# Performance work log

Measured on AMD Instinct MI355X. Metric: run time of the kernel, lower is better.

The kernel has to match this reference:

```python
import jax, jax.numpy as jnp
import numpy as np

N, E, D, H, C, G, L = 100000, 1600000, 128, 4, 32, 4096, 3  # nodes, edges, h_dim, heads, head_dim, graphs, conv blocks


def setup_inputs() -> dict:
    key = jax.random.key(0)
    ks = jax.random.split(key, 24)
    s = 0.05
    w = lambda k, shape: jax.random.normal(k, shape, jnp.float32) * s
    inp = {
        "x": jax.random.normal(ks[0], (N, D), jnp.float32),
        "edge_index": jax.random.randint(ks[1], (2, E), 0, N),
        "batch": jnp.sort(jax.random.randint(ks[2], (N,), 0, G)),
        # input TransformerConv (in=D, out=C per head, H heads, beta=True)
        "in_Wq": w(ks[3], (D, D)), "in_bq": jnp.zeros((D,), jnp.float32),
        "in_Wk": w(ks[4], (D, D)), "in_bk": jnp.zeros((D,), jnp.float32),
        "in_Wv": w(ks[5], (D, D)), "in_bv": jnp.zeros((D,), jnp.float32),
        "in_Ws": w(ks[6], (D, D)), "in_bs": jnp.zeros((D,), jnp.float32),
        "in_Wbeta": w(ks[7], (3 * D,)),
        # stacked conv blocks (L of them, in=out=D)
        "blk_Wq": w(ks[8], (L, D, D)), "blk_bq": jnp.zeros((L, D), jnp.float32),
        "blk_Wk": w(ks[9], (L, D, D)), "blk_bk": jnp.zeros((L, D), jnp.float32),
        "blk_Wv": w(ks[10], (L, D, D)), "blk_bv": jnp.zeros((L, D), jnp.float32),
        "blk_Ws": w(ks[11], (L, D, D)), "blk_bs": jnp.zeros((L, D), jnp.float32),
        "blk_Wbeta": w(ks[12], (L, 3 * D)),
        # MLP head
        "W1": w(ks[13], (D, 64)), "b1": jnp.zeros((64,), jnp.float32),
        "W2": w(ks[14], (64, 32)), "b2": jnp.zeros((32,), jnp.float32),
        "W3": w(ks[15], (32, 1)), "b3": jnp.zeros((1,), jnp.float32),
    }
    return inp


def transformer_conv(x, src, dst, Wq, bq, Wk, bk, Wv, bv, Ws, bs, Wbeta):
    # PyG TransformerConv, concat=True, root_weight=True, beta=True, eval mode
    q = (x @ Wq + bq).reshape(N, H, C)
    k = (x @ Wk + bk).reshape(N, H, C)
    v = (x @ Wv + bv).reshape(N, H, C)
    # per-edge attention logits: message j=src -> i=dst
    alpha = jnp.einsum("ehc,ehc->eh", q[dst], k[src]) / jnp.sqrt(jnp.float32(C))  # [E,H]
    m = jax.ops.segment_max(alpha, dst, num_segments=N)
    m = jnp.where(jnp.isfinite(m), m, 0.0)
    e = jnp.exp(alpha - m[dst])
    denom = jax.ops.segment_sum(e, dst, num_segments=N)
    a = e / (denom[dst] + 1e-16)  # segment softmax over in-edges of dst
    msg = a[..., None] * v[src]  # [E,H,C]
    out = jax.ops.segment_sum(msg, dst, num_segments=N).reshape(N, H * C)
    x_r = x @ Ws + bs
    beta = jax.nn.sigmoid(jnp.concatenate([out, x_r, out - x_r], axis=-1) @ Wbeta)[:, None]
    return beta * x_r + (1.0 - beta) * out


def reference(x, edge_index, batch, in_Wq, in_bq, in_Wk, in_bk, in_Wv, in_bv,
              in_Ws, in_bs, in_Wbeta, blk_Wq, blk_bq, blk_Wk, blk_bk, blk_Wv,
              blk_bv, blk_Ws, blk_bs, blk_Wbeta, W1, b1, W2, b2, W3, b3):
    src, dst = edge_index[0], edge_index[1]
    h = jax.nn.relu(transformer_conv(x, src, dst, in_Wq, in_bq, in_Wk, in_bk,
                                     in_Wv, in_bv, in_Ws, in_bs, in_Wbeta))
    for l in range(L):  # dropout is identity in eval mode
        h = jax.nn.relu(transformer_conv(h, src, dst, blk_Wq[l], blk_bq[l],
                                         blk_Wk[l], blk_bk[l], blk_Wv[l], blk_bv[l],
                                         blk_Ws[l], blk_bs[l], blk_Wbeta[l]))
    # global mean pool over graphs
    sums = jax.ops.segment_sum(h, batch, num_segments=G)
    cnt = jax.ops.segment_sum(jnp.ones((N, 1), h.dtype), batch, num_segments=G)
    g = sums / jnp.maximum(cnt, 1.0)
    g = jax.nn.relu(g @ W1 + b1)
    g = jax.nn.relu(g @ W2 + b2)
    return jax.nn.sigmoid(g @ W3 + b3)
```

## Files before the change

### kernel.cpp

```cpp
#include <hip/hip_runtime.h>
#include <hip/hip_bf16.h>
#include <cstdint>

#define DH 128
#define NB 256
#define NBK 1024

typedef __attribute__((ext_vector_type(8))) short short8;
typedef __attribute__((ext_vector_type(4))) float floatx4;
typedef __attribute__((ext_vector_type(2))) float floatx2;

__device__ __forceinline__ float bflo(unsigned u) { return __uint_as_float(u << 16); }
__device__ __forceinline__ float bfhi(unsigned u) { return __uint_as_float(u & 0xffff0000u); }

__device__ __forceinline__ unsigned pk_bf16(float a, float b) {
  return ((unsigned)__bfloat16_as_ushort(__float2bfloat16(b)) << 16)
       | (unsigned)__bfloat16_as_ushort(__float2bfloat16(a));
}

template<int CTRL>
__device__ __forceinline__ float dpp_add(float x) {
  int y = __builtin_amdgcn_update_dpp(0, __float_as_int(x), CTRL, 0xf, 0xf, true);
  return x + __int_as_float(y);
}


__global__ void zero_i32(int* __restrict__ p, int n) {
  int i = blockIdx.x * 256 + threadIdx.x;
  if (i < n) p[i] = 0;
}


__global__ void cvt_bf16(const float* __restrict__ x, __hip_bfloat16* __restrict__ o, int n) {
  int i = blockIdx.x * 256 + threadIdx.x;
  if (i < n) o[i] = __float2bfloat16(x[i]);
}


__global__ void hist_kernel(const int* __restrict__ dst, int* __restrict__ deg, int E) {
  int e = blockIdx.x * 256 + threadIdx.x;
  if (e < E) atomicAdd(&deg[dst[e]], 1);
}

__global__ void scan1_kernel(const int* __restrict__ deg, int* __restrict__ off,
                             int* __restrict__ bsum, int n) {
  __shared__ int sh[256];
  int idx = blockIdx.x * 256 + threadIdx.x;
  int v = (idx < n) ? deg[idx] : 0;
  sh[threadIdx.x] = v;
  __syncthreads();
  for (int d = 1; d < 256; d <<= 1) {
    int x = (threadIdx.x >= (unsigned)d) ? sh[threadIdx.x - d] : 0;
    __syncthreads();
    sh[threadIdx.x] += x;
    __syncthreads();
  }
  if (idx < n) off[idx] = sh[threadIdx.x] - v;
  if (threadIdx.x == 255) bsum[blockIdx.x] = sh[255];
}

__global__ void scan2_kernel(int* __restrict__ bsum, int nb) {
  __shared__ int sh[512];
  int t = threadIdx.x;
  int v = (t < nb) ? bsum[t] : 0;
  sh[t] = v;
  __syncthreads();
  for (int d = 1; d < 512; d <<= 1) {
    int x = (t >= (unsigned)d) ? sh[t - d] : 0;
    __syncthreads();
    sh[t] += x;
    __syncthreads();
  }
  if (t < nb) bsum[t] = sh[t] - v;
}

__global__ void scan3_kernel(int* __restrict__ off, const int* __restrict__ bsum, int n) {
  int idx = blockIdx.x * 256 + threadIdx.x;
  if (idx < n) off[idx] += bsum[blockIdx.x];
}


__global__ __launch_bounds__(256)
void csr_p1(const int* __restrict__ dst, int* __restrict__ hist, int E, int chunk) {
  __shared__ int cnt[NBK];
  const int blk = blockIdx.x, tid = threadIdx.x;
  for (int c = tid; c < NBK; c += 256) cnt[c] = 0;
  __syncthreads();
  int base = blk * chunk;
  int end = base + chunk; if (end > E) end = E;
  for (int e = base + tid; e < end; e += 256) atomicAdd(&cnt[dst[e] >> 7], 1);
  __syncthreads();
  for (int c = tid; c < NBK; c += 256) hist[blk * NBK + c] = cnt[c];
}

__global__ __launch_bounds__(256)
void csr_p2(int* __restrict__ hist, int* __restrict__ total) {
  int b = blockIdx.x * 256 + threadIdx.x;
  int run = 0;
  for (int blk = 0; blk < NB; ++blk) {
    int v = hist[blk * NBK + b];
    hist[blk * NBK + b] = run;
    run += v;
  }
  total[b] = run;
}

__global__ __launch_bounds__(256)
void csr_p3(const int* __restrict__ src, const int* __restrict__ dst,
            const int* __restrict__ hist, const int* __restrict__ tstart,
            int* __restrict__ part, int E, int chunk) {
  __shared__ int cur[NBK];
  const int blk = blockIdx.x, tid = threadIdx.x;
  for (int c = tid; c < NBK; c += 256) cur[c] = hist[blk * NBK + c] + tstart[c];
  __syncthreads();
  int base = blk * chunk;
  int end = base + chunk; if (end > E) end = E;
  for (int e = base + tid; e < end; e += 256) {
    int d = dst[e];
    int b = d >> 7;
    int pos = atomicAdd(&cur[b], 1);
    part[pos] = (src[e] << 7) | (d & 127);
  }
}

__global__ __launch_bounds__(256)
void csr_p4(const int* __restrict__ part, const int* __restrict__ tstart,
            const int* __restrict__ total, int* __restrict__ deg,
            int* __restrict__ off, int* __restrict__ csr, int Nn) {
  __shared__ int lcnt[128], lscan[128], lcur[128];
  const int b = blockIdx.x, tid = threadIdx.x;
  const int p0 = tstart[b];
  const int m = total[b];
  if (tid < 128) lcnt[tid] = 0;
  __syncthreads();
  for (int k = tid; k < m; k += 256) atomicAdd(&lcnt[part[p0 + k] & 127], 1);
  __syncthreads();
  if (tid < 128) lscan[tid] = lcnt[tid];
  __syncthreads();
  for (int d = 1; d < 128; d <<= 1) {
    int v = 0;
    if (tid < 128 && tid >= d) v = lscan[tid - d];
    __syncthreads();
    if (tid < 128) lscan[tid] += v;
    __syncthreads();
  }
  if (tid < 128) {
    int ex = lscan[tid] - lcnt[tid];
    lcur[tid] = ex;
    int n = (b << 7) + tid;
    if (n < Nn) { deg[n] = lcnt[tid]; off[n] = p0 + ex; }
  }
  __syncthreads();
  for (int k = tid; k < m; k += 256) {
    int pk = part[p0 + k];
    int pos = p0 + atomicAdd(&lcur[pk & 127], 1);
    csr[pos] = pk >> 7;
  }
}


__global__ void pack_w_kernel(const float* __restrict__ Wq, const float* __restrict__ Wk,
                              const float* __restrict__ Wv, const float* __restrict__ Ws,
                              const float* __restrict__ bq, const float* __restrict__ bk,
                              const float* __restrict__ bv, const float* __restrict__ bs,
                              __hip_bfloat16* __restrict__ WT, float* __restrict__ bcat) {
  int idx = blockIdx.x * 256 + threadIdx.x;
  if (idx < 512 * DH) {
    int c = idx >> 7, k = idx & 127;
    int which = c >> 7, cc = c & 127;
    const float* W = (which == 0) ? Wq : (which == 1) ? Wk : (which == 2) ? Wv : Ws;
    WT[idx] = __float2bfloat16(W[k * DH + cc]);
    if (k == 0) {
      const float* b = (which == 0) ? bq : (which == 1) ? bk : (which == 2) ? bv : bs;
      bcat[c] = b[cc];
    }
  }
}


__global__ __launch_bounds__(256)
void gemm_qkvs(const short* __restrict__ Xb, const short* __restrict__ WT,
               const float* __restrict__ bc,
               unsigned int* __restrict__ qout,
               unsigned int* __restrict__ kvp,
               unsigned int* __restrict__ xrout, int Nn) {
  const int row0 = blockIdx.x * 64;
  const int tid = threadIdx.x;
  const int w = tid >> 6, lane = tid & 63, quad = lane >> 4, l16 = lane & 15;

  short8 xf[4][4];
#pragma unroll
  for (int nt = 0; nt < 4; ++nt) {
    int node = row0 + nt * 16 + l16; if (node >= Nn) node = Nn - 1;
#pragma unroll
    for (int kt = 0; kt < 4; ++kt)
      xf[nt][kt] = *(const short8*)&Xb[(size_t)node * 128 + kt * 32 + quad * 8];
  }

  if (w == 0 || w == 3) {
    unsigned int* outp = (w == 0) ? qout : xrout;
    const int mbase = (w == 0) ? 0 : 24;
#pragma unroll
    for (int i = 0; i < 8; ++i) {
      const int mt = mbase + i;
      short8 af[4];
#pragma unroll
      for (int kt = 0; kt < 4; ++kt)
        af[kt] = *(const short8*)&WT[(size_t)(mt * 16 + l16) * 128 + kt * 32 + quad * 8];
      float4 bias = *(const float4*)&bc[mt * 16 + quad * 4];
      const int wc = (i * 16 + quad * 4);
#pragma unroll
      for (int nt = 0; nt < 4; ++nt) {
        floatx4 acc = (floatx4){0.f, 0.f, 0.f, 0.f};
#pragma unroll
        for (int kt = 0; kt < 4; ++kt)
          acc = __builtin_amdgcn_mfma_f32_16x16x32_bf16(af[kt], xf[nt][kt], acc, 0, 0, 0);
        int node = row0 + nt * 16 + l16;
        if (node < Nn) {
          uint2 o;
          o.x = pk_bf16(acc[0] + bias.x, acc[1] + bias.y);
          o.y = pk_bf16(acc[2] + bias.z, acc[3] + bias.w);
          *(uint2*)&outp[(size_t)node * 64 + (wc >> 1)] = o;
        }
      }
    }
  } else {
    const int kb = 8 + (w - 1) * 4;
    const int vb = 16 + (w - 1) * 4;
#pragma unroll
    for (int i = 0; i < 4; ++i) {
      const int mk = kb + i, mv = vb + i;
      short8 afk[4], afv[4];
#pragma unroll
      for (int kt = 0; kt < 4; ++kt) {
        afk[kt] = *(const short8*)&WT[(size_t)(mk * 16 + l16) * 128 + kt * 32 + quad * 8];
        afv[kt] = *(const short8*)&WT[(size_t)(mv * 16 + l16) * 128 + kt * 32 + quad * 8];
      }
      float4 bk4 = *(const float4*)&bc[mk * 16 + quad * 4];
      float4 bv4 = *(const float4*)&bc[mv * 16 + quad * 4];
      const int krel = (w - 1) * 64 + i * 16 + quad * 4;
#pragma unroll
      for (int nt = 0; nt < 4; ++nt) {
        floatx4 ak = (floatx4){0.f, 0.f, 0.f, 0.f};
        floatx4 av = (floatx4){0.f, 0.f, 0.f, 0.f};
#pragma unroll
        for (int kt = 0; kt < 4; ++kt) {
          ak = __builtin_amdgcn_mfma_f32_16x16x32_bf16(afk[kt], xf[nt][kt], ak, 0, 0, 0);
          av = __builtin_amdgcn_mfma_f32_16x16x32_bf16(afv[kt], xf[nt][kt], av, 0, 0, 0);
        }
        int node = row0 + nt * 16 + l16;
        if (node < Nn) {
          int d0 = __builtin_amdgcn_cvt_pk_fp8_f32(ak[0] + bk4.x, ak[1] + bk4.y, 0, false);
          d0 = __builtin_amdgcn_cvt_pk_fp8_f32(av[0] + bv4.x, av[1] + bv4.y, d0, true);
          int d1 = __builtin_amdgcn_cvt_pk_fp8_f32(ak[2] + bk4.z, ak[3] + bk4.w, 0, false);
          d1 = __builtin_amdgcn_cvt_pk_fp8_f32(av[2] + bv4.z, av[3] + bv4.w, d1, true);
          uint2 o; o.x = (unsigned)d0; o.y = (unsigned)d1;
          *(uint2*)&kvp[(size_t)node * 64 + (krel >> 1)] = o;
        }
      }
    }
  }
}


__global__ __launch_bounds__(256)
void attn_kernel(unsigned int* __restrict__ q_h, const unsigned int* __restrict__ kvp,
                 const unsigned int* __restrict__ xrb, const int* __restrict__ off,
                 const int* __restrict__ deg, const int* __restrict__ csr,
                 const float* __restrict__ Wb, int Nn) {
  int wv = __builtin_amdgcn_readfirstlane(threadIdx.x >> 6);
  int i = blockIdx.x * 4 + wv;
  if (i >= Nn) return;
  int l = threadIdx.x & 63;

  unsigned qp = q_h[(size_t)i * 64 + l];
  float q0 = bflo(qp), q1 = bfhi(qp);
  int e0 = off[i], e1 = e0 + deg[i];

  float den0 = 0.f, x00 = 0.f, x10 = 0.f;
  float den1 = 0.f, x01 = 0.f, x11 = 0.f;
  float den2 = 0.f, x02 = 0.f, x12 = 0.f;
  float den3 = 0.f, x03 = 0.f, x13 = 0.f;

  auto body = [&](int e, float& den, float& a0, float& a1) {
    int s = csr[e];
    int kq = (int)kvp[(size_t)s * 64 + l];
    floatx2 kk = __builtin_amdgcn_cvt_pk_f32_fp8(kq, false);
    floatx2 vv = __builtin_amdgcn_cvt_pk_f32_fp8(kq, true);
    float d = q0 * kk.x + q1 * kk.y;
    d = dpp_add<0x128>(d);
    d = dpp_add<0x124>(d);
    d = dpp_add<0x122>(d);
    d = dpp_add<0x121>(d);
    float p = __expf(d * 0.17677669529663687f);
    den += p; a0 += p * vv.x; a1 += p * vv.y;
  };

  int e = e0;
  for (; e + 3 < e1; e += 4) {
    body(e + 0, den0, x00, x10);
    body(e + 1, den1, x01, x11);
    body(e + 2, den2, x02, x12);
    body(e + 3, den3, x03, x13);
  }
  for (; e < e1; ++e) body(e, den0, x00, x10);

  float denom = den0 + den1 + den2 + den3 + 1e-16f;
  float o0 = (x00 + x01 + x02 + x03) / denom;
  float o1 = (x10 + x11 + x12 + x13) / denom;

  unsigned xp = xrb[(size_t)i * 64 + l];
  float xr0 = bflo(xp), xr1 = bfhi(xp);

  float c = o0 * Wb[2 * l] + o1 * Wb[2 * l + 1]
          + xr0 * Wb[128 + 2 * l] + xr1 * Wb[128 + 2 * l + 1]
          + (o0 - xr0) * Wb[256 + 2 * l] + (o1 - xr1) * Wb[256 + 2 * l + 1];
  c += __shfl_xor(c, 1);
  c += __shfl_xor(c, 2);
  c += __shfl_xor(c, 4);
  c += __shfl_xor(c, 8);
  c += __shfl_xor(c, 16);
  c += __shfl_xor(c, 32);
  float beta = 1.f / (1.f + __expf(-c));
  float h0 = fmaxf(beta * xr0 + (1.f - beta) * o0, 0.f);
  float h1 = fmaxf(beta * xr1 + (1.f - beta) * o1, 0.f);
  q_h[(size_t)i * 64 + l] = pk_bf16(h0, h1);
}


__global__ __launch_bounds__(128)
void poolmlp_kernel(const unsigned short* __restrict__ h, const int* __restrict__ goff,
                    const int* __restrict__ gdeg,
                    const float* __restrict__ W1, const float* __restrict__ b1,
                    const float* __restrict__ W2, const float* __restrict__ b2,
                    const float* __restrict__ W3, const float* __restrict__ b3,
                    float* __restrict__ out) {
  int g = blockIdx.x;
  int t = threadIdx.x;
  int n0 = goff[g], cnt = gdeg[g];
  float s = 0.f;
  for (int n = n0; n < n0 + cnt; ++n) s += bflo(h[(size_t)n * 128 + t]);
  __shared__ float gv[128];
  __shared__ float t1[64];
  __shared__ float t2[32];
  gv[t] = s / fmaxf((float)cnt, 1.0f);
  __syncthreads();
  if (t < 64) {
    float a = b1[t];
    for (int k = 0; k < 128; ++k) a += gv[k] * W1[k * 64 + t];
    t1[t] = fmaxf(a, 0.f);
  }
  __syncthreads();
  if (t < 32) {
    float a = b2[t];
    for (int k = 0; k < 64; ++k) a += t1[k] * W2[k * 32 + t];
    t2[t] = fmaxf(a, 0.f);
  }
  __syncthreads();
  if (t == 0) {
    float a = b3[0];
    for (int k = 0; k < 32; ++k) a += t2[k] * W3[k];
    out[g] = 1.f / (1.f + __expf(-a));
  }
}


extern "C" void kernel_launch(void* const* d_in, const int* in_sizes, int n_in,
                              void* d_out, int out_size, void* d_ws, size_t ws_size,
                              hipStream_t stream) {
  const float* x = (const float*)d_in[0];
  const int* edge_index = (const int*)d_in[1];
  const int* batch = (const int*)d_in[2];
  const int N = in_sizes[0] / DH;
  const int E = in_sizes[1] / 2;
  const int G = out_size;
  const int* src = edge_index;
  const int* dst = edge_index + E;

  const float* in_Wq = (const float*)d_in[3];
  const float* in_bq = (const float*)d_in[4];
  const float* in_Wk = (const float*)d_in[5];
  const float* in_bk = (const float*)d_in[6];
  const float* in_Wv = (const float*)d_in[7];
  const float* in_bv = (const float*)d_in[8];
  const float* in_Ws = (const float*)d_in[9];
  const float* in_bs = (const float*)d_in[10];
  const float* in_Wbeta = (const float*)d_in[11];
  const float* blk_Wq = (const float*)d_in[12];
  const float* blk_bq = (const float*)d_in[13];
  const float* blk_Wk = (const float*)d_in[14];
  const float* blk_bk = (const float*)d_in[15];
  const float* blk_Wv = (const float*)d_in[16];
  const float* blk_bv = (const float*)d_in[17];
  const float* blk_Ws = (const float*)d_in[18];
  const float* blk_bs = (const float*)d_in[19];
  const float* blk_Wbeta = (const float*)d_in[20];

  char* p = (char*)d_ws;
  auto take = [&](size_t bytes) { char* r = p; p += (bytes + 255) & ~(size_t)255; return r; };
  __hip_bfloat16* h0 = (__hip_bfloat16*)take((size_t)N * DH * 2);
  __hip_bfloat16* h1 = (__hip_bfloat16*)take((size_t)N * DH * 2);
  unsigned char* kvp = (unsigned char*)take((size_t)N * 256);
  unsigned short* xr = (unsigned short*)take((size_t)N * DH * 2);
  __hip_bfloat16* WT = (__hip_bfloat16*)take((size_t)512 * DH * 2);
  float* bcat = (float*)take(512 * 4);
  int* deg    = (int*)take((size_t)N * 4);
  int* off    = (int*)take((size_t)N * 4);
  int* csr    = (int*)take((size_t)E * 4);
  int* part   = (int*)take((size_t)E * 4);
  int* hist   = (int*)take((size_t)NB * NBK * 4);
  int* total  = (int*)take(NBK * 4);
  int* tstart = (int*)take(NBK * 4);
  int* bsumP  = (int*)take(512 * 4);
  int* gdeg   = (int*)take((size_t)G * 4);
  int* goff   = (int*)take((size_t)G * 4);
  int* bsum2  = (int*)take(512 * 4);
  (void)n_in;
  if ((size_t)(p - (char*)d_ws) > ws_size) return;

  const int NBUCK = (N + 127) >> 7;
  const int chunk = (E + NB - 1) / NB;
  int nb = (N + 255) / 256;
  int gb = (G + 255) / 256;

  csr_p1<<<NB, 256, 0, stream>>>(dst, hist, E, chunk);
  csr_p2<<<NBK / 256, 256, 0, stream>>>(hist, total);
  scan1_kernel<<<NBK / 256, 256, 0, stream>>>(total, tstart, bsumP, NBK);
  scan2_kernel<<<1, 512, 0, stream>>>(bsumP, NBK / 256);
  scan3_kernel<<<NBK / 256, 256, 0, stream>>>(tstart, bsumP, NBK);
  csr_p3<<<NB, 256, 0, stream>>>(src, dst, hist, tstart, part, E, chunk);
  csr_p4<<<NBUCK, 256, 0, stream>>>(part, tstart, total, deg, off, csr, N);

  zero_i32<<<gb, 256, 0, stream>>>(gdeg, G);
  hist_kernel<<<nb, 256, 0, stream>>>(batch, gdeg, N);
  scan1_kernel<<<gb, 256, 0, stream>>>(gdeg, goff, bsum2, G);
  scan2_kernel<<<1, 512, 0, stream>>>(bsum2, gb);
  scan3_kernel<<<gb, 256, 0, stream>>>(goff, bsum2, G);

  cvt_bf16<<<(int)(((size_t)N * DH + 255) / 256), 256, 0, stream>>>(x, h0, N * DH);

  for (int l = 0; l < 4; ++l) {
    const float *Wq, *Wk, *Wv, *Ws, *bq, *bk, *bv, *bs, *Wb;
    if (l == 0) {
      Wq = in_Wq; Wk = in_Wk; Wv = in_Wv; Ws = in_Ws;
      bq = in_bq; bk = in_bk; bv = in_bv; bs = in_bs; Wb = in_Wbeta;
    } else {
      int m = l - 1;
      Wq = blk_Wq + (size_t)m * DH * DH; Wk = blk_Wk + (size_t)m * DH * DH;
      Wv = blk_Wv + (size_t)m * DH * DH; Ws = blk_Ws + (size_t)m * DH * DH;
      bq = blk_bq + (size_t)m * DH; bk = blk_bk + (size_t)m * DH;
      bv = blk_bv + (size_t)m * DH; bs = blk_bs + (size_t)m * DH;
      Wb = blk_Wbeta + (size_t)m * 3 * DH;
    }
    __hip_bfloat16* hin  = (l & 1) ? h1 : h0;
    __hip_bfloat16* qbuf = (l & 1) ? h0 : h1;
    pack_w_kernel<<<(512 * DH + 255) / 256, 256, 0, stream>>>(Wq, Wk, Wv, Ws, bq, bk, bv, bs, WT, bcat);
    gemm_qkvs<<<(N + 63) / 64, 256, 0, stream>>>((const short*)hin, (const short*)WT, bcat,
        (unsigned int*)qbuf, (unsigned int*)kvp, (unsigned int*)xr, N);
    attn_kernel<<<(N + 3) / 4, 256, 0, stream>>>((unsigned int*)qbuf, (const unsigned int*)kvp,
        (const unsigned int*)xr, off, deg, csr, Wb, N);
  }

  poolmlp_kernel<<<G, 128, 0, stream>>>((const unsigned short*)h0, goff, gdeg,
      (const float*)d_in[21], (const float*)d_in[22],
      (const float*)d_in[23], (const float*)d_in[24],
      (const float*)d_in[25], (const float*)d_in[26],
      (float*)d_out);
}
```

Before: 790.2 us.

## Process four edges per wave with 16-byte KV loads in attention kernel

The attention kernel now splits each wave into four 16-lane groups. Each group handles a different edge and each lane covers 8 features through 16-byte loads of fp8 K/V and bf16 q. The GEMM epilogue reorders the packed fp8 K/V bytes to match the new per-lane layout. The q scale and log2e are folded into q so exp2f can be used, and group partials are reduced with cross-group shuffles at the end. This aims to raise memory-level parallelism per gather and to cut the per-edge DPP reduction chain, at the cost of predicated tail iterations and extra registers.

New measurement: 827.3 us. +4.7%, slower.

```diff
diff --git a/kernel.cpp b/kernel.cpp
--- a/kernel.cpp
+++ b/kernel.cpp
@@ -16,12 +16,6 @@
 __device__ __forceinline__ unsigned pk_bf16(float a, float b) {
   return ((unsigned)__bfloat16_as_ushort(__float2bfloat16(b)) << 16)
        | (unsigned)__bfloat16_as_ushort(__float2bfloat16(a));
-}
-
-template<int CTRL>
-__device__ __forceinline__ float dpp_add(float x) {
-  int y = __builtin_amdgcn_update_dpp(0, __float_as_int(x), CTRL, 0xf, 0xf, true);
-  return x + __int_as_float(y);
 }
 
 
@@ -251,8 +245,8 @@
         int node = row0 + nt * 16 + l16;
         if (node < Nn) {
           int d0 = __builtin_amdgcn_cvt_pk_fp8_f32(ak[0] + bk4.x, ak[1] + bk4.y, 0, false);
-          d0 = __builtin_amdgcn_cvt_pk_fp8_f32(av[0] + bv4.x, av[1] + bv4.y, d0, true);
-          int d1 = __builtin_amdgcn_cvt_pk_fp8_f32(ak[2] + bk4.z, ak[3] + bk4.w, 0, false);
+          d0 = __builtin_amdgcn_cvt_pk_fp8_f32(ak[2] + bk4.z, ak[3] + bk4.w, d0, true);
+          int d1 = __builtin_amdgcn_cvt_pk_fp8_f32(av[0] + bv4.x, av[1] + bv4.y, 0, false);
           d1 = __builtin_amdgcn_cvt_pk_fp8_f32(av[2] + bv4.z, av[3] + bv4.w, d1, true);
           uint2 o; o.x = (unsigned)d0; o.y = (unsigned)d1;
           *(uint2*)&kvp[(size_t)node * 64 + (krel >> 1)] = o;
@@ -264,67 +258,112 @@
 
 
 __global__ __launch_bounds__(256)
-void attn_kernel(unsigned int* __restrict__ q_h, const unsigned int* __restrict__ kvp,
-                 const unsigned int* __restrict__ xrb, const int* __restrict__ off,
+void attn_kernel(unsigned int* __restrict__ q_h, const uint4* __restrict__ kvp4,
+                 const uint4* __restrict__ xr4, const int* __restrict__ off,
                  const int* __restrict__ deg, const int* __restrict__ csr,
                  const float* __restrict__ Wb, int Nn) {
   int wv = __builtin_amdgcn_readfirstlane(threadIdx.x >> 6);
   int i = blockIdx.x * 4 + wv;
   if (i >= Nn) return;
   int l = threadIdx.x & 63;
-
-  unsigned qp = q_h[(size_t)i * 64 + l];
-  float q0 = bflo(qp), q1 = bfhi(qp);
+  int t16 = l & 15;
+  int g = l >> 4;
+
+  const float QS = 0.17677669529663687f * 1.4426950408889634f;
+  uint4 qw = ((const uint4*)q_h)[(size_t)i * 16 + t16];
+  float q0 = bflo(qw.x) * QS, q1 = bfhi(qw.x) * QS;
+  float q2 = bflo(qw.y) * QS, q3 = bfhi(qw.y) * QS;
+  float q4 = bflo(qw.z) * QS, q5 = bfhi(qw.z) * QS;
+  float q6 = bflo(qw.w) * QS, q7 = bfhi(qw.w) * QS;
+
   int e0 = off[i], e1 = e0 + deg[i];
 
-  float den0 = 0.f, x00 = 0.f, x10 = 0.f;
-  float den1 = 0.f, x01 = 0.f, x11 = 0.f;
-  float den2 = 0.f, x02 = 0.f, x12 = 0.f;
-  float den3 = 0.f, x03 = 0.f, x13 = 0.f;
-
-  auto body = [&](int e, float& den, float& a0, float& a1) {
-    int s = csr[e];
-    int kq = (int)kvp[(size_t)s * 64 + l];
-    floatx2 kk = __builtin_amdgcn_cvt_pk_f32_fp8(kq, false);
-    floatx2 vv = __builtin_amdgcn_cvt_pk_f32_fp8(kq, true);
-    float d = q0 * kk.x + q1 * kk.y;
-    d = dpp_add<0x128>(d);
-    d = dpp_add<0x124>(d);
-    d = dpp_add<0x122>(d);
-    d = dpp_add<0x121>(d);
-    float p = __expf(d * 0.17677669529663687f);
-    den += p; a0 += p * vv.x; a1 += p * vv.y;
+  float denA = 0.f, denB = 0.f;
+  float aA[8] = {0.f,0.f,0.f,0.f,0.f,0.f,0.f,0.f};
+  float aB[8] = {0.f,0.f,0.f,0.f,0.f,0.f,0.f,0.f};
+
+  auto body = [&](int e, float& den, float (&acc)[8]) {
+    bool valid = e < e1;
+    int ec = valid ? e : e1 - 1;
+    int s = csr[ec];
+    uint4 kv = kvp4[(size_t)s * 16 + t16];
+    floatx2 k01 = __builtin_amdgcn_cvt_pk_f32_fp8((int)kv.x, false);
+    floatx2 k23 = __builtin_amdgcn_cvt_pk_f32_fp8((int)kv.x, true);
+    floatx2 k45 = __builtin_amdgcn_cvt_pk_f32_fp8((int)kv.z, false);
+    floatx2 k67 = __builtin_amdgcn_cvt_pk_f32_fp8((int)kv.z, true);
+    floatx2 v01 = __builtin_amdgcn_cvt_pk_f32_fp8((int)kv.y, false);
+    floatx2 v23 = __builtin_amdgcn_cvt_pk_f32_fp8((int)kv.y, true);
+    floatx2 v45 = __builtin_amdgcn_cvt_pk_f32_fp8((int)kv.w, false);
+    floatx2 v67 = __builtin_amdgcn_cvt_pk_f32_fp8((int)kv.w, true);
+    float d = q0 * k01.x + q1 * k01.y + q2 * k23.x + q3 * k23.y
+            + q4 * k45.x + q5 * k45.y + q6 * k67.x + q7 * k67.y;
+    d += __shfl_xor(d, 1);
+    d += __shfl_xor(d, 2);
+    float p = exp2f(d);
+    p = valid ? p : 0.f;
+    den += p;
+    acc[0] += p * v01.x; acc[1] += p * v01.y;
+    acc[2] += p * v23.x; acc[3] += p * v23.y;
+    acc[4] += p * v45.x; acc[5] += p * v45.y;
+    acc[6] += p * v67.x; acc[7] += p * v67.y;
   };
 
-  int e = e0;
-  for (; e + 3 < e1; e += 4) {
-    body(e + 0, den0, x00, x10);
-    body(e + 1, den1, x01, x11);
-    body(e + 2, den2, x02, x12);
-    body(e + 3, den3, x03, x13);
-  }
-  for (; e < e1; ++e) body(e, den0, x00, x10);
-
-  float denom = den0 + den1 + den2 + den3 + 1e-16f;
-  float o0 = (x00 + x01 + x02 + x03) / denom;
-  float o1 = (x10 + x11 + x12 + x13) / denom;
-
-  unsigned xp = xrb[(size_t)i * 64 + l];
-  float xr0 = bflo(xp), xr1 = bfhi(xp);
-
-  float c = o0 * Wb[2 * l] + o1 * Wb[2 * l + 1]
-          + xr0 * Wb[128 + 2 * l] + xr1 * Wb[128 + 2 * l + 1]
-          + (o0 - xr0) * Wb[256 + 2 * l] + (o1 - xr1) * Wb[256 + 2 * l + 1];
+  int nIt = (e1 - e0 + 7) >> 3;
+  int eA = e0 + g, eB = e0 + g + 4;
+  for (int it = 0; it < nIt; ++it) {
+    body(eA, denA, aA);
+    body(eB, denB, aB);
+    eA += 8; eB += 8;
+  }
+
+  float den = denA + denB;
+  den += __shfl_xor(den, 16);
+  den += __shfl_xor(den, 32);
+  float inv = 1.f / (den + 1e-16f);
+  float o[8];
+#pragma unroll
+  for (int f = 0; f < 8; ++f) {
+    float a = aA[f] + aB[f];
+    a += __shfl_xor(a, 16);
+    a += __shfl_xor(a, 32);
+    o[f] = a * inv;
+  }
+
+  uint4 xw = xr4[(size_t)i * 16 + t16];
+  float xr[8];
+  xr[0] = bflo(xw.x); xr[1] = bfhi(xw.x);
+  xr[2] = bflo(xw.y); xr[3] = bfhi(xw.y);
+  xr[4] = bflo(xw.z); xr[5] = bfhi(xw.z);
+  xr[6] = bflo(xw.w); xr[7] = bfhi(xw.w);
+
+  int f0 = t16 * 8;
+  float4 wo0 = *(const float4*)&Wb[f0];
+  float4 wo1 = *(const float4*)&Wb[f0 + 4];
+  float4 wx0 = *(const float4*)&Wb[128 + f0];
+  float4 wx1 = *(const float4*)&Wb[128 + f0 + 4];
+  float4 wd0 = *(const float4*)&Wb[256 + f0];
+  float4 wd1 = *(const float4*)&Wb[256 + f0 + 4];
+  float c = o[0]*wo0.x + o[1]*wo0.y + o[2]*wo0.z + o[3]*wo0.w
+          + o[4]*wo1.x + o[5]*wo1.y + o[6]*wo1.z + o[7]*wo1.w
+          + xr[0]*wx0.x + xr[1]*wx0.y + xr[2]*wx0.z + xr[3]*wx0.w
+          + xr[4]*wx1.x + xr[5]*wx1.y + xr[6]*wx1.z + xr[7]*wx1.w
+          + (o[0]-xr[0])*wd0.x + (o[1]-xr[1])*wd0.y + (o[2]-xr[2])*wd0.z + (o[3]-xr[3])*wd0.w
+          + (o[4]-xr[4])*wd1.x + (o[5]-xr[5])*wd1.y + (o[6]-xr[6])*wd1.z + (o[7]-xr[7])*wd1.w;
   c += __shfl_xor(c, 1);
   c += __shfl_xor(c, 2);
   c += __shfl_xor(c, 4);
   c += __shfl_xor(c, 8);
-  c += __shfl_xor(c, 16);
-  c += __shfl_xor(c, 32);
   float beta = 1.f / (1.f + __expf(-c));
-  float h0 = fmaxf(beta * xr0 + (1.f - beta) * o0, 0.f);
-  float h1 = fmaxf(beta * xr1 + (1.f - beta) * o1, 0.f);
-  q_h[(size_t)i * 64 + l] = pk_bf16(h0, h1);
+
+  if (g == 0) {
+    float h[8];
+#pragma unroll
+    for (int f = 0; f < 8; ++f) h[f] = fmaxf(beta * xr[f] + (1.f - beta) * o[f], 0.f);
+    uint4 hw;
+    hw.x = pk_bf16(h[0], h[1]); hw.y = pk_bf16(h[2], h[3]);
+    hw.z = pk_bf16(h[4], h[5]); hw.w = pk_bf16(h[6], h[7]);
+    ((uint4*)q_h)[(size_t)i * 16 + t16] = hw;
+  }
 }
 
 
@@ -457,8 +496,8 @@
     pack_w_kernel<<<(512 * DH + 255) / 256, 256, 0, stream>>>(Wq, Wk, Wv, Ws, bq, bk, bv, bs, WT, bcat);
     gemm_qkvs<<<(N + 63) / 64, 256, 0, stream>>>((const short*)hin, (const short*)WT, bcat,
         (unsigned int*)qbuf, (unsigned int*)kvp, (unsigned int*)xr, N);
-    attn_kernel<<<(N + 3) / 4, 256, 0, stream>>>((unsigned int*)qbuf, (const unsigned int*)kvp,
-        (const unsigned int*)xr, off, deg, csr, Wb, N);
+    attn_kernel<<<(N + 3) / 4, 256, 0, stream>>>((unsigned int*)qbuf, (const uint4*)kvp,
+        (const uint4*)xr, off, deg, csr, Wb, N);
   }
 
   poolmlp_kernel<<<G, 128, 0, stream>>>((const unsigned short*)h0, goff, gdeg,
```
